# Performance work log

Measured on AMD Instinct MI355X. Metric: run time of the kernel, lower is better.

The kernel has to match this reference:

```python
import jax, jax.numpy as jnp
import numpy as np

EPS_BN = 1e-5

def _grid_sample(fea, gx, gy):
    # fea: [B,C,H,W]; gx,gy: [B,P] normalized to [-1,1]; bilinear, zeros padding, align_corners=True
    B, C, H, W = fea.shape
    x = (gx + 1.0) * 0.5 * (W - 1)
    y = (gy + 1.0) * 0.5 * (H - 1)
    x0 = jnp.floor(x)
    y0 = jnp.floor(y)
    wx1 = x - x0
    wy1 = y - y0
    flat = fea.reshape(B, C, H * W)
    def tap(xi, yi, w):
        valid = ((xi >= 0) & (xi <= W - 1) & (yi >= 0) & (yi <= H - 1)).astype(fea.dtype)
        xi_c = jnp.clip(xi, 0, W - 1).astype(jnp.int32)
        yi_c = jnp.clip(yi, 0, H - 1).astype(jnp.int32)
        g = jnp.take_along_axis(flat, (yi_c * W + xi_c)[:, None, :], axis=2)  # [B,C,P]
        return g * (w * valid)[:, None, :]
    return (tap(x0, y0, (1 - wx1) * (1 - wy1)) + tap(x0 + 1, y0, wx1 * (1 - wy1))
            + tap(x0, y0 + 1, (1 - wx1) * wy1) + tap(x0 + 1, y0 + 1, wx1 * wy1))

def _homo_warp(src_fea, src_proj, ref_proj, depth_values):
    # src_fea: [B,C,H,W] -> warped [B,C,D,H,W] (MVSNet homo_warping, grid under stop_gradient)
    B, C, H, W = src_fea.shape
    D = depth_values.shape[1]
    proj = jnp.matmul(src_proj, jnp.linalg.inv(ref_proj))
    rot, trans = proj[:, :3, :3], proj[:, :3, 3]
    yy, xx = jnp.meshgrid(jnp.arange(H, dtype=src_fea.dtype), jnp.arange(W, dtype=src_fea.dtype), indexing='ij')
    xyz = jnp.stack([xx.ravel(), yy.ravel(), jnp.ones(H * W, src_fea.dtype)], 0)  # [3,HW]
    rot_xyz = jnp.einsum('bij,jp->bip', rot, xyz)  # [B,3,HW]
    pxyz = rot_xyz[:, :, None, :] * depth_values.reshape(B, 1, D, H * W) + trans[:, :, None, None]  # [B,3,D,HW]
    z = pxyz[:, 2]
    gx = jax.lax.stop_gradient(((pxyz[:, 0] / z) / ((W - 1) / 2.0) - 1.0).reshape(B, D * H * W))
    gy = jax.lax.stop_gradient(((pxyz[:, 1] / z) / ((H - 1) / 2.0) - 1.0).reshape(B, D * H * W))
    return _grid_sample(src_fea, gx, gy).reshape(B, C, D, H, W)

def _pixelwise_net(x, w0, g0, b0, m0, v0, w1, g1, b1, m1, v1, w2, b2):
    # x: [B,1,D,H,W]; 1x1x1 Conv3d(bias=False)+BN+ReLU twice, then Conv3d(8->1)+sigmoid+max over D
    def bnrelu(h, g, b, m, v):
        s = (1, -1, 1, 1, 1)
        return jax.nn.relu((h - m.reshape(s)) * (g / jnp.sqrt(v + EPS_BN)).reshape(s) + b.reshape(s))
    h = bnrelu(jnp.einsum('oc,bcdhw->bodhw', w0, x), g0, b0, m0, v0)
    h = bnrelu(jnp.einsum('oc,bcdhw->bodhw', w1, h), g1, b1, m1, v1)
    h = jnp.einsum('oc,bcdhw->bodhw', w2, h) + b2.reshape(1, -1, 1, 1, 1)
    out = jax.nn.sigmoid(h[:, 0])  # [B,D,H,W]
    return jnp.max(out, axis=1, keepdims=True)  # [B,1,H,W]

def _forward(features, proj_matrices, depth_values, num_depth,
             pw_w0, pw_g0, pw_b0, pw_m0, pw_v0, pw_w1, pw_g1, pw_b1, pw_m1, pw_v1, pw_w2, pw_b2,
             reg_w, reg_b):
    ref_fea = features[0]
    B, C, H, W = ref_fea.shape
    V = features.shape[0]
    D = num_depth
    def proj_new(p):  # p: [B,2,4,4] -> K @ E on top 3 rows
        top = jnp.matmul(p[:, 1, :3, :3], p[:, 0, :3, :4])
        return jnp.concatenate([top, p[:, 0, 3:4, :]], axis=1)
    ref_proj_new = proj_new(proj_matrices[:, 0])
    sim_sum = jnp.zeros((B, 1, D, H, W), ref_fea.dtype)
    w_sum = jnp.full((B, 1, 1, H, W), 1e-5, ref_fea.dtype)
    vw_list = []
    for i in range(1, V):  # small fixed loop over source views
        src_proj_new = proj_new(proj_matrices[:, i])
        warped = _homo_warp(features[i], src_proj_new, ref_proj_new, depth_values)
        sim = jnp.mean(warped * ref_fea[:, :, None], axis=1, keepdims=True)  # [B,1,D,H,W]
        vw = _pixelwise_net(sim, pw_w0, pw_g0, pw_b0, pw_m0, pw_v0, pw_w1, pw_g1, pw_b1, pw_m1, pw_v1, pw_w2, pw_b2)
        vw_list.append(vw)
        sim_sum = sim_sum + sim * vw[:, :, None]
        w_sum = w_sum + vw[:, :, None]
    similarity = sim_sum / w_sum
    cost_reg = jax.lax.conv_general_dilated(similarity, reg_w, (1, 1, 1), 'SAME',
                                            dimension_numbers=('NCDHW', 'OIDHW', 'NCDHW')) + reg_b.reshape(1, -1, 1, 1, 1)
    prob_volume = jax.nn.softmax(cost_reg[:, 0], axis=1)  # exp(log_softmax) == softmax
    idx = jnp.argmax(prob_volume, axis=1, keepdims=True)
    depth = jnp.take_along_axis(depth_values, idx, axis=1)[:, 0]  # WTA depth [B,H,W]
    conf = jnp.max(prob_volume, axis=1)
    view_weights = jnp.concatenate(vw_list, axis=1)
    return depth, conf, prob_volume, cost_reg, view_weights

def setup_inputs():
    key = jax.random.key(0)
    ks = jax.random.split(key, 20)
    B, V, C, H, W, D = 2, 5, 32, 128, 160, 32
    features = jax.random.normal(ks[0], (V, B, C, H, W), jnp.float32)
    K = np.eye(4, dtype=np.float32)
    K[0, 0] = 180.0; K[1, 1] = 180.0; K[0, 2] = W / 2.0; K[1, 2] = H / 2.0
    pm = np.zeros((B, V, 2, 4, 4), np.float32)
    for v in range(V):
        E = np.eye(4, dtype=np.float32)
        E[0, 3] = 10.0 * v  # horizontal baseline per source view
        pm[:, v, 0] = E
        pm[:, v, 1] = K
    depth_values = jnp.broadcast_to(jnp.linspace(425.0, 935.0, D, dtype=jnp.float32)[None, :, None, None], (B, D, H, W)) + 0.0
    rn = lambda k, s, sc=0.3: jax.random.normal(k, s, jnp.float32) * sc
    return {
        'features': features,
        'proj_matrices': jnp.asarray(pm),
        'depth_values': depth_values,
        'num_depth': D,
        'pw_w0': rn(ks[1], (16, 1)),
        'pw_g0': 1.0 + rn(ks[2], (16,), 0.1), 'pw_b0': rn(ks[3], (16,), 0.1),
        'pw_m0': rn(ks[4], (16,), 0.1), 'pw_v0': 1.0 + 0.5 * jax.random.uniform(ks[5], (16,)),
        'pw_w1': rn(ks[6], (8, 16)),
        'pw_g1': 1.0 + rn(ks[7], (8,), 0.1), 'pw_b1': rn(ks[8], (8,), 0.1),
        'pw_m1': rn(ks[9], (8,), 0.1), 'pw_v1': 1.0 + 0.5 * jax.random.uniform(ks[10], (8,)),
        'pw_w2': rn(ks[11], (1, 8)),
        'pw_b2': rn(ks[12], (1,), 0.1),
        'reg_w': rn(ks[13], (1, 1, 3, 3, 3), 0.1),
        'reg_b': rn(ks[14], (1,), 0.1),
    }

def reference(features, proj_matrices, depth_values, num_depth,
              pw_w0, pw_g0, pw_b0, pw_m0, pw_v0, pw_w1, pw_g1, pw_b1, pw_m1, pw_v1, pw_w2, pw_b2,
              reg_w, reg_b):
    return _forward(features, proj_matrices, depth_values, num_depth,
                    pw_w0, pw_g0, pw_b0, pw_m0, pw_v0, pw_w1, pw_g1, pw_b1, pw_m1, pw_v1, pw_w2, pw_b2,
                    reg_w, reg_b)
```

## Files before the change

### kernel.cpp

```cpp
#include <hip/hip_runtime.h>
#include <math.h>

#define BB 2
#define VV 5
#define CC 32
#define HH 128
#define WW 160
#define DD 32
#define HWp (HH*WW)
#define NV (VV-1)
#define PX 16
#define MAXSLOT 18
#define UWMAX 30

#define OFF_RT   0
#define OFF_PRM  96
#define OFF_FEAT 512
#define OFF_SIM  (OFF_FEAT + VV*BB*HWp*CC)
#define OFF_T    (OFF_SIM + BB*DD*HWp)
#define OFF_TAB  (OFF_T + 16)
#define OFF_FLAG (OFF_TAB + 17*16)

#define OUT_DEPTH 0
#define OUT_CONF  (BB*HWp)
#define OUT_PROB  (2*BB*HWp)
#define OUT_COST  (OUT_PROB + BB*DD*HWp)
#define OUT_VW    (OUT_COST + BB*DD*HWp)

#define ZI(d,k)     smemU[(d)*17 + (k)]
#define DEP(d,k)    smemU[(d)*17 + (k)]
#define REF(p,c)    smemU[544 + (p)*36 + (c)]
#define GT(v,p,i)   smemU[1120 + ((v)*16 + (p))*18 + (i)]
#define AY0(v,p)    smemU[2272 + (v)*16 + (p)]
#define AY1(v,p)    smemU[2336 + (v)*16 + (p)]
#define IR0(v,p)    smemI[2400 + (v)*16 + (p)]
#define IR1(v,p)    smemI[2464 + (v)*16 + (p)]
#define IXB(v,p)    smemI[2528 + (v)*16 + (p)]
#define ISL(v,p)    smemI[2592 + (v)*16 + (p)]
#define BADF        smemI[2656]
#define SIMG(v,d,p) smemU[544 + (((v)*32 + (d))*17 + (p))]
#define COLU(v,ux,c) smemU[2720 + (v)*(UWMAX*36) + (ux)*36 + (c)]
#define UOKI(v)     smemI[7040 + (v)]
#define UXLOI(v)    smemI[7044 + (v)]
#define UWI(v)      smemI[7048 + (v)]

__device__ void build_proj(const float* proj, int b, int v, double M[4][4]) {
    const float* E = proj + (((b*VV + v)*2 + 0)*16);
    const float* K = proj + (((b*VV + v)*2 + 1)*16);
    for (int r = 0; r < 3; r++)
        for (int c = 0; c < 4; c++) {
            double s = 0.0;
            for (int k = 0; k < 3; k++) s += (double)K[r*4+k] * (double)E[k*4+c];
            M[r][c] = s;
        }
    for (int c = 0; c < 4; c++) M[3][c] = (double)E[12+c];
}

__device__ void inv4(const double M[4][4], double out[4][4]) {
    double a[4][8];
    for (int i = 0; i < 4; i++)
        for (int j = 0; j < 4; j++) { a[i][j] = M[i][j]; a[i][4+j] = (i == j) ? 1.0 : 0.0; }
    for (int col = 0; col < 4; col++) {
        int piv = col; double best = fabs(a[col][col]);
        for (int r = col+1; r < 4; r++) if (fabs(a[r][col]) > best) { best = fabs(a[r][col]); piv = r; }
        if (piv != col) for (int j = 0; j < 8; j++) { double t = a[col][j]; a[col][j] = a[piv][j]; a[piv][j] = t; }
        double dinv = 1.0 / a[col][col];
        for (int j = 0; j < 8; j++) a[col][j] *= dinv;
        for (int r = 0; r < 4; r++) {
            if (r == col) continue;
            double f = a[r][col];
            for (int j = 0; j < 8; j++) a[r][j] -= f * a[col][j];
        }
    }
    for (int i = 0; i < 4; i++) for (int j = 0; j < 4; j++) out[i][j] = a[i][4+j];
}

__device__ void setup_body(const float* __restrict__ proj,
    const float* __restrict__ w0, const float* __restrict__ g0, const float* __restrict__ b0,
    const float* __restrict__ m0, const float* __restrict__ v0,
    const float* __restrict__ w1, const float* __restrict__ g1, const float* __restrict__ b1,
    const float* __restrict__ m1, const float* __restrict__ v1,
    const float* __restrict__ w2, const float* __restrict__ b2,
    float* __restrict__ ws, int t,
    float* __restrict__ prmL, float* __restrict__ TL) {

    if (t < BB*NV) {
        int b = t / NV, v = 1 + (t % NV);
        double refM[4][4], inv[4][4], S[4][4];
        build_proj(proj, b, 0, refM);
        inv4(refM, inv);
        build_proj(proj, b, v, S);
        float* rt = ws + OFF_RT + (b*NV + (v-1))*12;
        for (int r = 0; r < 3; r++) {
            for (int c = 0; c < 3; c++) {
                double s = 0.0;
                for (int k = 0; k < 4; k++) s += S[r][k] * inv[k][c];
                rt[r*3 + c] = (float)s;
            }
            double s = 0.0;
            for (int k = 0; k < 4; k++) s += S[r][k] * inv[k][3];
            rt[9 + r] = (float)s;
        }
    }

    if (t < 16) {
        float sc = g0[t] / sqrtf(v0[t] + 1e-5f);
        prmL[t]      = w0[t] * sc;
        prmL[16 + t] = b0[t] - m0[t] * sc;
    }
    if (t >= 32 && t < 160) {
        int i = t - 32, q = i >> 4, o = i & 15;
        float sc = g1[q] / sqrtf(v1[q] + 1e-5f);
        prmL[32 + q*16 + o] = w1[q*16 + o] * sc;
    }
    if (t >= 160 && t < 168) {
        int q = t - 160;
        float sc = g1[q] / sqrtf(v1[q] + 1e-5f);
        prmL[160 + q] = b1[q] - m1[q] * sc;
        prmL[168 + q] = w2[q];
    }
    if (t == 176) prmL[176] = b2[0];
    __syncthreads();

    if (t < BB) {
        int ok = 1;
        for (int i = 0; i < NV; i++) {
            const float* ri = ws + OFF_RT + (t*NV + i)*12;
            ok &= (fabsf(ri[6])        < 1e-6f);
            ok &= (fabsf(ri[7])        < 1e-6f);
            ok &= (fabsf(ri[8] - 1.f)  < 1e-6f);
            ok &= (fabsf(ri[10])       < 1e-6f);
            ok &= (fabsf(ri[11])       < 1e-6f);
        }
        ws[OFF_FLAG + t] = ok ? 1.f : 0.f;
    }

    if (t == 0) {
        float tmp[16]; int nk = 0;
        for (int o = 0; o < 16; o++) {
            float a = prmL[o];
            if (a != 0.f) tmp[nk++] = -prmL[16+o] / a;
        }
        for (int i = 1; i < nk; i++) {
            float key = tmp[i]; int j = i-1;
            while (j >= 0 && tmp[j] > key) { tmp[j+1] = tmp[j]; j--; }
            tmp[j+1] = key;
        }
        for (int i = 0; i < 16; i++) TL[i] = (i < nk) ? tmp[i] : 3.4e38f;
    }
    __syncthreads();

    if (t < 17*8) {
        int seg = t >> 3, q = t & 7;
        float lo = (seg == 0)  ? -1e30f : TL[seg-1];
        float hi = (seg == 16) ?  1e30f : TL[seg];
        float smid;
        if (hi > 1e29f)       smid = lo + 1.f;
        else if (lo < -1e29f) smid = hi - 1.f;
        else                  smid = 0.5f*(lo + hi);
        float alpha = 0.f, beta = prmL[160+q];
        #pragma unroll
        for (int o = 0; o < 16; o++) {
            float a = prmL[o], c = prmL[16+o];
            if (a*smid + c > 0.f) {
                alpha += prmL[32+q*16+o]*a;
                beta  += prmL[32+q*16+o]*c;
            }
        }
        ws[OFF_TAB + seg*16 + q]     = alpha;
        ws[OFF_TAB + seg*16 + 8 + q] = beta;
    }
    if (t < 177) ws[OFF_PRM + t] = prmL[t];
    if (t < 16)  ws[OFF_T + t]   = TL[t];
}

__global__ __launch_bounds__(256) void transpose_setup_kernel(
    const float* __restrict__ fea, float* __restrict__ featT,
    const float* __restrict__ proj,
    const float* __restrict__ w0, const float* __restrict__ g0, const float* __restrict__ b0,
    const float* __restrict__ m0, const float* __restrict__ v0,
    const float* __restrict__ w1, const float* __restrict__ g1, const float* __restrict__ b1,
    const float* __restrict__ m1, const float* __restrict__ v1,
    const float* __restrict__ w2, const float* __restrict__ b2,
    float* __restrict__ ws) {
    __shared__ float prmL[177];
    __shared__ float TL[16];
    if (blockIdx.x == 0)
        setup_body(proj, w0, g0, b0, m0, v0, w1, g1, b1, m1, v1, w2, b2,
                   ws, threadIdx.x, prmL, TL);

    int t = blockIdx.x*256 + threadIdx.x;
    int w = t % WW;
    int h = (t / WW) % HH;
    int b = (t / (WW*HH)) % BB;
    int v = t / (WW*HH*BB);
    const float* src = fea + (size_t)((v*BB + b)*CC) * HWp + h*WW + w;
    float* dst = featT + (size_t)((v*BB + b)*HWp + h*WW + w) * CC;
    #pragma unroll
    for (int c = 0; c < CC; c += 4) {
        float4 q;
        q.x = src[(c+0)*HWp];
        q.y = src[(c+1)*HWp];
        q.z = src[(c+2)*HWp];
        q.w = src[(c+3)*HWp];
        *reinterpret_cast<float4*>(dst + c) = q;
    }
}

__device__ __forceinline__ float half_max(float v) {
    v = fmaxf(v, __shfl_xor(v, 1));
    v = fmaxf(v, __shfl_xor(v, 2));
    v = fmaxf(v, __shfl_xor(v, 4));
    v = fmaxf(v, __shfl_xor(v, 8));
    v = fmaxf(v, __shfl_xor(v, 16));
    return v;
}

__device__ __forceinline__ float dot32(const float* __restrict__ col,
                                       const float* __restrict__ refp) {
    float acc = 0.f;
    #pragma unroll
    for (int c = 0; c < CC; c += 4) {
        float4 a = *reinterpret_cast<const float4*>(col + c);
        float4 r = *reinterpret_cast<const float4*>(refp + c);
        acc = fmaf(a.w, r.w, fmaf(a.z, r.z, fmaf(a.y, r.y, fmaf(a.x, r.x, acc))));
    }
    return acc;
}

__device__ __forceinline__ float dot32_lds(const float* __restrict__ col,
                                           const float* __restrict__ refp) {
    float acc = 0.f;
    #pragma unroll
    for (int c = 0; c < CC; c += 4) {
        float4 a = *reinterpret_cast<const float4*>(col + c);
        float4 r = *reinterpret_cast<const float4*>(refp + c);
        acc = fmaf(a.w, r.w, fmaf(a.z, r.z, fmaf(a.y, r.y, fmaf(a.x, r.x, acc))));
    }
    return acc;
}

__device__ __forceinline__ void mlp_out(
    float s0, float s1, float s2, float s3,
    int d2, int b, int p,
    const float* __restrict__ tabL, const float* __restrict__ Tg,
    const float* __restrict__ prm,
    float* __restrict__ out, float* __restrict__ simout) {
    float T0 = Tg[0], T1 = Tg[1], T2 = Tg[2], T3 = Tg[3];
    float T4 = Tg[4], T5 = Tg[5], T6 = Tg[6], T7 = Tg[7];
    float T8 = Tg[8], T9 = Tg[9], T10 = Tg[10], T11 = Tg[11];
    float T12 = Tg[12], T13 = Tg[13], T14 = Tg[14], T15 = Tg[15];
    float wq0 = prm[168], wq1 = prm[169], wq2 = prm[170], wq3 = prm[171];
    float wq4 = prm[172], wq5 = prm[173], wq6 = prm[174], wq7 = prm[175];
    float p176 = prm[176];

    float sv[NV] = {s0, s1, s2, s3};
    float vw[NV];
    #pragma unroll
    for (int v = 0; v < NV; v++) {
        float s = sv[v];
        int seg = 0;
        seg += (s > T0);  seg += (s > T1);  seg += (s > T2);  seg += (s > T3);
        seg += (s > T4);  seg += (s > T5);  seg += (s > T6);  seg += (s > T7);
        seg += (s > T8);  seg += (s > T9);  seg += (s > T10); seg += (s > T11);
        seg += (s > T12); seg += (s > T13); seg += (s > T14); seg += (s > T15);
        const float* row = &tabL[seg << 4];
        float4 A0 = *reinterpret_cast<const float4*>(row);
        float4 A1 = *reinterpret_cast<const float4*>(row + 4);
        float4 B0 = *reinterpret_cast<const float4*>(row + 8);
        float4 B1 = *reinterpret_cast<const float4*>(row + 12);
        float h2v = p176;
        h2v = fmaf(wq0, fmaxf(fmaf(A0.x, s, B0.x), 0.f), h2v);
        h2v = fmaf(wq1, fmaxf(fmaf(A0.y, s, B0.y), 0.f), h2v);
        h2v = fmaf(wq2, fmaxf(fmaf(A0.z, s, B0.z), 0.f), h2v);
        h2v = fmaf(wq3, fmaxf(fmaf(A0.w, s, B0.w), 0.f), h2v);
        h2v = fmaf(wq4, fmaxf(fmaf(A1.x, s, B1.x), 0.f), h2v);
        h2v = fmaf(wq5, fmaxf(fmaf(A1.y, s, B1.y), 0.f), h2v);
        h2v = fmaf(wq6, fmaxf(fmaf(A1.z, s, B1.z), 0.f), h2v);
        h2v = fmaf(wq7, fmaxf(fmaf(A1.w, s, B1.w), 0.f), h2v);
        float m = half_max(h2v);
        vw[v] = 1.f/(1.f + __expf(-m));
    }

    if (d2 == 0) out[OUT_VW + (b*NV + 0)*HWp + p] = vw[0];
    if (d2 == 1) out[OUT_VW + (b*NV + 1)*HWp + p] = vw[1];
    if (d2 == 2) out[OUT_VW + (b*NV + 2)*HWp + p] = vw[2];
    if (d2 == 3) out[OUT_VW + (b*NV + 3)*HWp + p] = vw[3];

    float wsum = 1e-5f + vw[0] + vw[1] + vw[2] + vw[3];
    float ssum = s0*vw[0] + s1*vw[1] + s2*vw[2] + s3*vw[3];
    simout[(b*DD + d2)*HWp + p] = ssum / wsum;
}

__device__ __forceinline__ float tap_blend(
    const float* __restrict__ vbv, int sub8, float sx,
    float ay0, float ay1, int r0, int r1,
    float4 rva, float4 rvb) {
    float x0f = floorf(sx);
    float wx1 = sx - x0f;
    float wx0 = 1.f - wx1;
    int xi0 = (int)x0f, xi1 = xi0 + 1;
    float ax0 = ((unsigned)xi0 < WW) ? wx0 : 0.f;
    float ax1 = ((unsigned)xi1 < WW) ? wx1 : 0.f;
    int xc0 = min(max(xi0, 0), WW-1);
    int xc1 = min(max(xi1, 0), WW-1);
    float w00 = ax0*ay0, w01 = ax1*ay0;
    const float* q00 = vbv + (((r0 + xc0) << 5) + sub8);
    const float* q01 = vbv + (((r0 + xc1) << 5) + sub8);
    float4 t00a = *reinterpret_cast<const float4*>(q00);
    float4 t00b = *reinterpret_cast<const float4*>(q00 + 4);
    float4 t01a = *reinterpret_cast<const float4*>(q01);
    float4 t01b = *reinterpret_cast<const float4*>(q01 + 4);

    float blx = fmaf(w01, t01a.x, w00*t00a.x);
    float bly = fmaf(w01, t01a.y, w00*t00a.y);
    float blz = fmaf(w01, t01a.z, w00*t00a.z);
    float blw = fmaf(w01, t01a.w, w00*t00a.w);
    float acc = fmaf(rva.w,blw, fmaf(rva.z,blz, fmaf(rva.y,bly, rva.x*blx)));
    blx = fmaf(w01, t01b.x, w00*t00b.x);
    bly = fmaf(w01, t01b.y, w00*t00b.y);
    blz = fmaf(w01, t01b.z, w00*t00b.z);
    blw = fmaf(w01, t01b.w, w00*t00b.w);
    acc = fmaf(rvb.w,blw, fmaf(rvb.z,blz, fmaf(rvb.y,bly, fmaf(rvb.x,blx, acc))));

    if (ay1 != 0.f) {
        float w10 = ax0*ay1, w11 = ax1*ay1;
        const float* q10 = vbv + (((r1 + xc0) << 5) + sub8);
        const float* q11 = vbv + (((r1 + xc1) << 5) + sub8);
        float4 t10a = *reinterpret_cast<const float4*>(q10);
        float4 t10b = *reinterpret_cast<const float4*>(q10 + 4);
        float4 t11a = *reinterpret_cast<const float4*>(q11);
        float4 t11b = *reinterpret_cast<const float4*>(q11 + 4);
        float cx = fmaf(w11, t11a.x, w10*t10a.x);
        float cy = fmaf(w11, t11a.y, w10*t10a.y);
        float cz = fmaf(w11, t11a.z, w10*t10a.z);
        float cw = fmaf(w11, t11a.w, w10*t10a.w);
        acc = fmaf(rva.w,cw, fmaf(rva.z,cz, fmaf(rva.y,cy, fmaf(rva.x,cx, acc))));
        cx = fmaf(w11, t11b.x, w10*t10b.x);
        cy = fmaf(w11, t11b.y, w10*t10b.y);
        cz = fmaf(w11, t11b.z, w10*t10b.z);
        cw = fmaf(w11, t11b.w, w10*t10b.w);
        acc = fmaf(rvb.w,cw, fmaf(rvb.z,cz, fmaf(rvb.y,cy, fmaf(rvb.x,cx, acc))));
    }
    return acc;
}

__global__ __launch_bounds__(256) void fused_sim_kernel(
    const float* __restrict__ featT, const float* __restrict__ rtAll,
    const float* __restrict__ prm, const float* __restrict__ Tg,
    const float* __restrict__ tabG, const float* __restrict__ flagG,
    const float* __restrict__ depthv,
    float* __restrict__ simout, float* __restrict__ out) {
    __shared__ __align__(16) float smemU[7056];
    __shared__ __align__(16) float tabL[17*16];
    int* smemI = (int*)smemU;

    int t = threadIdx.x;
    int b = blockIdx.y;
    int pbase = blockIdx.x * PX;
    int hi  = pbase / WW;
    int wi0 = pbase % WW;
    float fy = (float)hi;

    bool fast = (flagG[b] != 0.f);

    {
        int di = t >> 4, k = t & 15;
        float dep0 = depthv[(b*DD + di)*HWp + pbase + k];
        float dep1 = depthv[(b*DD + di + 16)*HWp + pbase + k];
        if (fast) {
            ZI(di, k)    = __builtin_amdgcn_rcpf(dep0);
            ZI(di+16, k) = __builtin_amdgcn_rcpf(dep1);
            if (t < 128) {
                int p = t >> 3, c4 = (t & 7) * 4;
                float4 rq = *reinterpret_cast<const float4*>(
                    featT + (size_t)(b*HWp + pbase + p)*CC + c4);
                *reinterpret_cast<float4*>(&REF(p, c4)) = rq;
            }
        } else {
            DEP(di, k)    = dep0;
            DEP(di+16, k) = dep1;
        }
        tabL[t] = tabG[t];
        if (t < 16) tabL[256 + t] = tabG[256 + t];
        if (t == 0 && fast) BADF = 0;
    }
    __syncthreads();

    float rc[NV][12];
    #pragma unroll
    for (int v = 0; v < NV; v++)
        #pragma unroll
        for (int j = 0; j < 12; j++)
            rc[v][j] = rtAll[(b*NV + v)*12 + j];
    float bx0[NV], by0[NV], bz0[NV];
    #pragma unroll
    for (int v = 0; v < NV; v++) {
        bx0[v] = fmaf((float)wi0, rc[v][0], fmaf(fy, rc[v][1], rc[v][2]));
        by0[v] = fmaf((float)wi0, rc[v][3], fmaf(fy, rc[v][4], rc[v][5]));
        bz0[v] = fmaf((float)wi0, rc[v][6], fmaf(fy, rc[v][7], rc[v][8]));
    }

    bool needRestage = false;
    if (fast) {
        int p_loc = t >> 5, d = t & 31;
        for (int ph = 0; ph < 2; ph++) {
            int p = ph*8 + p_loc;
            float zi = ZI(d, p);
            float mnz = zi, mxz = zi;
            #pragma unroll
            for (int off = 1; off <= 16; off <<= 1) {
                mnz = fminf(mnz, __shfl_xor(mnz, off));
                mxz = fmaxf(mxz, __shfl_xor(mxz, off));
            }
            if (d == 0) {
                float fk = (float)p;
                #pragma unroll
                for (int v = 0; v < NV; v++) {
                    float bx = fmaf(fk, rc[v][0], bx0[v]);
                    float t0c = rc[v][9];
                    float sxa = fmaf(t0c, mnz, bx);
                    float sxb = fmaf(t0c, mxz, bx);
                    float mn = fminf(sxa, sxb), mx = fmaxf(sxa, sxb);
                    float by = fmaf(fk, rc[v][3], by0[v]);
                    float sy = by;
                    float sny = rintf(sy);
                    sy = (fabsf(sy - sny) < 1e-4f) ? sny : sy;
                    float y0f = floorf(sy);
                    float wy1 = sy - y0f, wy0 = 1.f - wy1;
                    int yi0 = (int)y0f, yi1 = yi0 + 1;
                    AY0(v, p) = ((unsigned)yi0 < HH) ? wy0 : 0.f;
                    AY1(v, p) = ((unsigned)yi1 < HH) ? wy1 : 0.f;
                    IR0(v, p) = min(max(yi0, 0), HH-1)*WW;
                    IR1(v, p) = min(max(yi1, 0), HH-1)*WW;
                    bool finite = (mn > -1e9f) && (mx < 1e9f) && (mn == mn) && (mx == mx);
                    int xb = finite ? (int)floorf(mn) : 0;
                    int slots = finite ? ((int)floorf(mx) - xb + 2) : MAXSLOT + 1;
                    IXB(v, p) = xb;
                    ISL(v, p) = slots;
                    if (slots > MAXSLOT) BADF = 1;
                }
            }
        }
        __syncthreads();
        if (BADF) { fast = false; needRestage = true; }
    }

    bool uni = false;
    if (fast) {
        if (t < 64) {
            int v = t >> 4, p = t & 15;
            int ok = (AY1(v, p) == 0.f) && (IR0(v, p) == IR0(v, 0)) ? 1 : 0;
            int xlo = IXB(v, p);
            int xhi = xlo + ISL(v, p) - 1;
            #pragma unroll
            for (int off = 1; off <= 8; off <<= 1) {
                ok  &= __shfl_xor(ok, off);
                xlo  = min(xlo, __shfl_xor(xlo, off));
                xhi  = max(xhi, __shfl_xor(xhi, off));
            }
            if (p == 0) {
                int wdt = xhi - xlo + 1;
                UOKI(v)  = (ok && wdt <= UWMAX) ? 1 : 0;
                UXLOI(v) = xlo;
                UWI(v)   = wdt;
            }
        }
        __syncthreads();
        uni = UOKI(0) && UOKI(1) && UOKI(2) && UOKI(3);
    }

    if (fast) {
        if (uni) {
            for (int i = t; i < NV*UWMAX*8; i += 256) {
                int v  = i / (UWMAX*8);
                int rem = i - v*(UWMAX*8);
                int ux = rem >> 3, c4 = (rem & 7) * 4;
                if (ux < UWI(v)) {
                    int xc = min(max(UXLOI(v) + ux, 0), WW-1);
                    int r0 = IR0(v, 0);
                    const float* src = featT + (size_t)(((v+1)*BB + b)*HWp)*CC
                                       + ((r0 + xc) << 5) + c4;
                    float4 q = *reinterpret_cast<const float4*>(src);
                    *reinterpret_cast<float4*>(&COLU(v, ux, c4)) = q;
                }
            }
            __syncthreads();
            {
                int v2 = t & 3, p2 = (t >> 2) & 15, i0 = t >> 6;
                float ay0 = AY0(v2, p2);
                int xb = IXB(v2, p2), slots = ISL(v2, p2);
                int xoff = xb - UXLOI(v2);
                const float* refp = &REF(p2, 0);
                for (int i2 = i0; i2 < slots; i2 += 4) {
                    const float* col = &COLU(v2, xoff + i2, 0);
                    float g = ay0 * dot32_lds(col, refp);
                    GT(v2, p2, i2) = g * (1.f/(float)CC);
                }
            }
            __syncthreads();
        } else {
            {
                int v2 = t & 3, p2 = (t >> 2) & 15, i0 = t >> 6;
                float ay0 = AY0(v2, p2), ay1 = AY1(v2, p2);
                int r0 = IR0(v2, p2), r1 = IR1(v2, p2);
                int xb = IXB(v2, p2), slots = ISL(v2, p2);
                const float* vbv = featT + (size_t)(((v2+1)*BB + b)*HWp)*CC;
                const float* refp = &REF(p2, 0);
                for (int i2 = i0; i2 < slots; i2 += 4) {
                    int xc = min(max(xb + i2, 0), WW-1);
                    float g = ay0 * dot32(vbv + ((r0 + xc) << 5), refp);
                    if (ay1 != 0.f) g = fmaf(ay1, dot32(vbv + ((r1 + xc) << 5), refp), g);
                    GT(v2, p2, i2) = g * (1.f/(float)CC);
                }
            }
            __syncthreads();
        }
        {
            int p_loc = t >> 5, d = t & 31;
            for (int ph = 0; ph < 2; ph++) {
                int p = ph*8 + p_loc;
                float fk = (float)p;
                float zi = ZI(d, p);
                float sv[NV];
                #pragma unroll
                for (int v = 0; v < NV; v++) {
                    float bx = fmaf(fk, rc[v][0], bx0[v]);
                    float sx = fmaf(rc[v][9], zi, bx);
                    float x0f = floorf(sx);
                    float wx1 = sx - x0f, wx0 = 1.f - wx1;
                    int xi0 = (int)x0f, xi1 = xi0 + 1;
                    float ax0 = ((unsigned)xi0 < WW) ? wx0 : 0.f;
                    float ax1 = ((unsigned)xi1 < WW) ? wx1 : 0.f;
                    int ii = xi0 - IXB(v, p);
                    float g0 = GT(v, p, ii);
                    float g1 = GT(v, p, ii+1);
                    sv[v] = fmaf(ax0, g0, ax1*g1);
                }
                mlp_out(sv[0], sv[1], sv[2], sv[3], d, b, pbase + p,
                        tabL, Tg, prm, out, simout);
            }
        }
        return;
    }

    if (needRestage) {
        int di = t >> 4, k = t & 15;
        DEP(di, k)    = depthv[(b*DD + di)*HWp + pbase + k];
        DEP(di+16, k) = depthv[(b*DD + di + 16)*HWp + pbase + k];
        __syncthreads();
    }
    {
        int sub = t & 3;
        int dB  = (t >> 2) & 31;
        int kk  = t >> 7;
        int sub8 = sub*8;
        #pragma unroll 2
        for (int j = 0; j < PX/2; j++) {
            int kpix = j*2 + kk;
            int p = pbase + kpix;
            float fk = (float)kpix;
            float depth = DEP(dB, kpix);
            const float* refp = featT + (size_t)(b*HWp + p)*CC + sub8;
            float4 rva = *reinterpret_cast<const float4*>(refp);
            float4 rvb = *reinterpret_cast<const float4*>(refp + 4);

            #pragma unroll
            for (int v = 0; v < NV; v++) {
                float bx = fmaf(fk, rc[v][0], bx0[v]);
                float by = fmaf(fk, rc[v][3], by0[v]);
                float bz = fmaf(fk, rc[v][6], bz0[v]);
                float px = fmaf(bx, depth, rc[v][9]);
                float py = fmaf(by, depth, rc[v][10]);
                float pz = fmaf(bz, depth, rc[v][11]);
                float zi = __builtin_amdgcn_rcpf(pz);
                float sx = px * zi, sy = py * zi;
                float sny = rintf(sy);
                sy = (fabsf(sy - sny) < 1e-4f) ? sny : sy;
                float y0f = floorf(sy);
                float wy1 = sy - y0f, wy0 = 1.f - wy1;
                int yi0 = (int)y0f, yi1 = yi0 + 1;
                float ay0 = ((unsigned)yi0 < HH) ? wy0 : 0.f;
                float ay1 = ((unsigned)yi1 < HH) ? wy1 : 0.f;
                int yc0 = min(max(yi0, 0), HH-1);
                int yc1 = min(max(yi1, 0), HH-1);
                int r0 = yc0*WW, r1 = yc1*WW;
                const float* vbv = featT + (size_t)(((v+1)*BB + b)*HWp)*CC;
                float acc = tap_blend(vbv, sub8, sx, ay0, ay1, r0, r1, rva, rvb);
                acc += __shfl_xor(acc, 1);
                acc += __shfl_xor(acc, 2);
                if (sub == 0) SIMG(v, dB, kpix) = acc * (1.f/(float)CC);
            }
        }
        __syncthreads();

        int p8 = t >> 5;
        int d2 = t & 31;
        #pragma unroll
        for (int pi = 0; pi < PX/8; pi++) {
            int pidx = pi*8 + p8;
            mlp_out(SIMG(0, d2, pidx), SIMG(1, d2, pidx),
                    SIMG(2, d2, pidx), SIMG(3, d2, pidx),
                    d2, b, pbase + pidx, tabL, Tg, prm, out, simout);
        }
    }
}

__global__ __launch_bounds__(256) void convsm_kernel(
    const float* __restrict__ sim, const float* __restrict__ rw,
    const float* __restrict__ rb, const float* __restrict__ depthv,
    float* __restrict__ out) {
    __shared__ float tile[34*121 + 7];
    int t = threadIdx.x;
    int tw = blockIdx.x * 8;
    int th = blockIdx.y * 8;
    int b  = blockIdx.z;

    for (int i = t; i < 34*120; i += 256) {
        int e = i / 120; int rem = i % 120;
        int h = rem / 12, w = rem % 12;
        int gd = e - 1, gh = th + h - 1, gw = tw + w - 1;
        float v = 0.f;
        if (w < 10 && gd >= 0 && gd < DD && (unsigned)gh < HH && (unsigned)gw < WW)
            v = sim[((b*DD + gd)*HH + gh)*WW + gw];
        tile[e*121 + rem] = v;
    }
    __syncthreads();

    float wk[27];
    #pragma unroll
    for (int i = 0; i < 27; i++) wk[i] = rw[i];
    float bias = rb[0];

    int p  = t >> 2, dq = t & 3;
    int ph = p >> 3, pw = p & 7;
    int d0 = dq * 8;

    float cost[8];
    #pragma unroll
    for (int j = 0; j < 8; j++) cost[j] = bias;
    #pragma unroll
    for (int e = 0; e < 10; e++) {
        int el = d0 + e;
        float s0 = 0.f, s1 = 0.f, s2 = 0.f;
        #pragma unroll
        for (int kh = 0; kh < 3; kh++) {
            #pragma unroll
            for (int kw = 0; kw < 3; kw++) {
                float x = tile[el*121 + (ph+kh)*12 + (pw+kw)];
                s0 = fmaf(wk[0*9 + kh*3 + kw], x, s0);
                s1 = fmaf(wk[1*9 + kh*3 + kw], x, s1);
                s2 = fmaf(wk[2*9 + kh*3 + kw], x, s2);
            }
        }
        if (e < 8)            cost[e]   += s0;
        if (e >= 1 && e <= 8) cost[e-1] += s1;
        if (e >= 2)           cost[e-2] += s2;
    }

    int pg = (th + ph)*WW + (tw + pw);
    #pragma unroll
    for (int j = 0; j < 8; j++)
        out[OUT_COST + (b*DD + d0 + j)*HWp + pg] = cost[j];

    float m = cost[0]; int mi = d0;
    #pragma unroll
    for (int j = 1; j < 8; j++) { if (cost[j] > m) { m = cost[j]; mi = d0 + j; } }
    #pragma unroll
    for (int off = 1; off <= 2; off <<= 1) {
        float m2 = __shfl_xor(m, off);
        int  i2 = __shfl_xor(mi, off);
        if (m2 > m || (m2 == m && i2 < mi)) { m = m2; mi = i2; }
    }
    float sum = 0.f;
    float e8[8];
    #pragma unroll
    for (int j = 0; j < 8; j++) { e8[j] = __expf(cost[j] - m); sum += e8[j]; }
    #pragma unroll
    for (int off = 1; off <= 2; off <<= 1) sum += __shfl_xor(sum, off);
    float inv = 1.f / sum;
    #pragma unroll
    for (int j = 0; j < 8; j++)
        out[OUT_PROB + (b*DD + d0 + j)*HWp + pg] = e8[j] * inv;
    if (dq == 0) {
        out[OUT_DEPTH + b*HWp + pg] = depthv[(b*DD + mi)*HWp + pg];
        out[OUT_CONF  + b*HWp + pg] = inv;
    }
}

extern "C" void kernel_launch(void* const* d_in, const int* in_sizes, int n_in,
                              void* d_out, int out_size, void* d_ws, size_t ws_size,
                              hipStream_t stream) {
    const float* features = (const float*)d_in[0];
    const float* proj     = (const float*)d_in[1];
    const float* depthv   = (const float*)d_in[2];
    const float* w0 = (const float*)d_in[4];
    const float* g0 = (const float*)d_in[5];
    const float* b0 = (const float*)d_in[6];
    const float* m0 = (const float*)d_in[7];
    const float* v0 = (const float*)d_in[8];
    const float* w1 = (const float*)d_in[9];
    const float* g1 = (const float*)d_in[10];
    const float* b1 = (const float*)d_in[11];
    const float* m1 = (const float*)d_in[12];
    const float* v1 = (const float*)d_in[13];
    const float* w2 = (const float*)d_in[14];
    const float* b2 = (const float*)d_in[15];
    const float* rw = (const float*)d_in[16];
    const float* rb = (const float*)d_in[17];
    float* out = (float*)d_out;
    float* ws  = (float*)d_ws;

    transpose_setup_kernel<<<VV*BB*HWp/256, 256, 0, stream>>>(
        features, ws + OFF_FEAT, proj,
        w0, g0, b0, m0, v0, w1, g1, b1, m1, v1, w2, b2, ws);

    fused_sim_kernel<<<dim3(HWp/PX, BB), 256, 0, stream>>>(
        ws + OFF_FEAT, ws + OFF_RT, ws + OFF_PRM, ws + OFF_T, ws + OFF_TAB,
        ws + OFF_FLAG, depthv, ws + OFF_SIM, out);

    convsm_kernel<<<dim3(WW/8, HH/8, BB), 256, 0, stream>>>(
        ws + OFF_SIM, rw, rb, depthv, out);
}
```

Baseline: 72.30 us.

## Drop feature transpose pass and gather directly from channel-major features

Result: slower. 81.36 us (+12.5%).

```diff
diff --git a/kernel.cpp b/kernel.cpp
--- a/kernel.cpp
+++ b/kernel.cpp
@@ -15,8 +15,7 @@
 
 #define OFF_RT   0
 #define OFF_PRM  96
-#define OFF_FEAT 512
-#define OFF_SIM  (OFF_FEAT + VV*BB*HWp*CC)
+#define OFF_SIM  512
 #define OFF_T    (OFF_SIM + BB*DD*HWp)
 #define OFF_TAB  (OFF_T + 16)
 #define OFF_FLAG (OFF_TAB + 17*16)
@@ -75,14 +74,16 @@
     for (int i = 0; i < 4; i++) for (int j = 0; j < 4; j++) out[i][j] = a[i][4+j];
 }
 
-__device__ void setup_body(const float* __restrict__ proj,
+__global__ __launch_bounds__(256) void setup_kernel(const float* __restrict__ proj,
     const float* __restrict__ w0, const float* __restrict__ g0, const float* __restrict__ b0,
     const float* __restrict__ m0, const float* __restrict__ v0,
     const float* __restrict__ w1, const float* __restrict__ g1, const float* __restrict__ b1,
     const float* __restrict__ m1, const float* __restrict__ v1,
     const float* __restrict__ w2, const float* __restrict__ b2,
-    float* __restrict__ ws, int t,
-    float* __restrict__ prmL, float* __restrict__ TL) {
+    float* __restrict__ ws) {
+    __shared__ float prmL[177];
+    __shared__ float TL[16];
+    int t = threadIdx.x;
 
     if (t < BB*NV) {
         int b = t / NV, v = 1 + (t % NV);
@@ -174,39 +175,6 @@
     if (t < 16)  ws[OFF_T + t]   = TL[t];
 }
 
-__global__ __launch_bounds__(256) void transpose_setup_kernel(
-    const float* __restrict__ fea, float* __restrict__ featT,
-    const float* __restrict__ proj,
-    const float* __restrict__ w0, const float* __restrict__ g0, const float* __restrict__ b0,
-    const float* __restrict__ m0, const float* __restrict__ v0,
-    const float* __restrict__ w1, const float* __restrict__ g1, const float* __restrict__ b1,
-    const float* __restrict__ m1, const float* __restrict__ v1,
-    const float* __restrict__ w2, const float* __restrict__ b2,
-    float* __restrict__ ws) {
-    __shared__ float prmL[177];
-    __shared__ float TL[16];
-    if (blockIdx.x == 0)
-        setup_body(proj, w0, g0, b0, m0, v0, w1, g1, b1, m1, v1, w2, b2,
-                   ws, threadIdx.x, prmL, TL);
-
-    int t = blockIdx.x*256 + threadIdx.x;
-    int w = t % WW;
-    int h = (t / WW) % HH;
-    int b = (t / (WW*HH)) % BB;
-    int v = t / (WW*HH*BB);
-    const float* src = fea + (size_t)((v*BB + b)*CC) * HWp + h*WW + w;
-    float* dst = featT + (size_t)((v*BB + b)*HWp + h*WW + w) * CC;
-    #pragma unroll
-    for (int c = 0; c < CC; c += 4) {
-        float4 q;
-        q.x = src[(c+0)*HWp];
-        q.y = src[(c+1)*HWp];
-        q.z = src[(c+2)*HWp];
-        q.w = src[(c+3)*HWp];
-        *reinterpret_cast<float4*>(dst + c) = q;
-    }
-}
-
 __device__ __forceinline__ float half_max(float v) {
     v = fmaxf(v, __shfl_xor(v, 1));
     v = fmaxf(v, __shfl_xor(v, 2));
@@ -214,18 +182,6 @@
     v = fmaxf(v, __shfl_xor(v, 8));
     v = fmaxf(v, __shfl_xor(v, 16));
     return v;
-}
-
-__device__ __forceinline__ float dot32(const float* __restrict__ col,
-                                       const float* __restrict__ refp) {
-    float acc = 0.f;
-    #pragma unroll
-    for (int c = 0; c < CC; c += 4) {
-        float4 a = *reinterpret_cast<const float4*>(col + c);
-        float4 r = *reinterpret_cast<const float4*>(refp + c);
-        acc = fmaf(a.w, r.w, fmaf(a.z, r.z, fmaf(a.y, r.y, fmaf(a.x, r.x, acc))));
-    }
-    return acc;
 }
 
 __device__ __forceinline__ float dot32_lds(const float* __restrict__ col,
@@ -292,61 +248,8 @@
     simout[(b*DD + d2)*HWp + p] = ssum / wsum;
 }
 
-__device__ __forceinline__ float tap_blend(
-    const float* __restrict__ vbv, int sub8, float sx,
-    float ay0, float ay1, int r0, int r1,
-    float4 rva, float4 rvb) {
-    float x0f = floorf(sx);
-    float wx1 = sx - x0f;
-    float wx0 = 1.f - wx1;
-    int xi0 = (int)x0f, xi1 = xi0 + 1;
-    float ax0 = ((unsigned)xi0 < WW) ? wx0 : 0.f;
-    float ax1 = ((unsigned)xi1 < WW) ? wx1 : 0.f;
-    int xc0 = min(max(xi0, 0), WW-1);
-    int xc1 = min(max(xi1, 0), WW-1);
-    float w00 = ax0*ay0, w01 = ax1*ay0;
-    const float* q00 = vbv + (((r0 + xc0) << 5) + sub8);
-    const float* q01 = vbv + (((r0 + xc1) << 5) + sub8);
-    float4 t00a = *reinterpret_cast<const float4*>(q00);
-    float4 t00b = *reinterpret_cast<const float4*>(q00 + 4);
-    float4 t01a = *reinterpret_cast<const float4*>(q01);
-    float4 t01b = *reinterpret_cast<const float4*>(q01 + 4);
-
-    float blx = fmaf(w01, t01a.x, w00*t00a.x);
-    float bly = fmaf(w01, t01a.y, w00*t00a.y);
-    float blz = fmaf(w01, t01a.z, w00*t00a.z);
-    float blw = fmaf(w01, t01a.w, w00*t00a.w);
-    float acc = fmaf(rva.w,blw, fmaf(rva.z,blz, fmaf(rva.y,bly, rva.x*blx)));
-    blx = fmaf(w01, t01b.x, w00*t00b.x);
-    bly = fmaf(w01, t01b.y, w00*t00b.y);
-    blz = fmaf(w01, t01b.z, w00*t00b.z);
-    blw = fmaf(w01, t01b.w, w00*t00b.w);
-    acc = fmaf(rvb.w,blw, fmaf(rvb.z,blz, fmaf(rvb.y,bly, fmaf(rvb.x,blx, acc))));
-
-    if (ay1 != 0.f) {
-        float w10 = ax0*ay1, w11 = ax1*ay1;
-        const float* q10 = vbv + (((r1 + xc0) << 5) + sub8);
-        const float* q11 = vbv + (((r1 + xc1) << 5) + sub8);
-        float4 t10a = *reinterpret_cast<const float4*>(q10);
-        float4 t10b = *reinterpret_cast<const float4*>(q10 + 4);
-        float4 t11a = *reinterpret_cast<const float4*>(q11);
-        float4 t11b = *reinterpret_cast<const float4*>(q11 + 4);
-        float cx = fmaf(w11, t11a.x, w10*t10a.x);
-        float cy = fmaf(w11, t11a.y, w10*t10a.y);
-        float cz = fmaf(w11, t11a.z, w10*t10a.z);
-        float cw = fmaf(w11, t11a.w, w10*t10a.w);
-        acc = fmaf(rva.w,cw, fmaf(rva.z,cz, fmaf(rva.y,cy, fmaf(rva.x,cx, acc))));
-        cx = fmaf(w11, t11b.x, w10*t10b.x);
-        cy = fmaf(w11, t11b.y, w10*t10b.y);
-        cz = fmaf(w11, t11b.z, w10*t10b.z);
-        cw = fmaf(w11, t11b.w, w10*t10b.w);
-        acc = fmaf(rvb.w,cw, fmaf(rvb.z,cz, fmaf(rvb.y,cy, fmaf(rvb.x,cx, acc))));
-    }
-    return acc;
-}
-
 __global__ __launch_bounds__(256) void fused_sim_kernel(
-    const float* __restrict__ featT, const float* __restrict__ rtAll,
+    const float* __restrict__ fea, const float* __restrict__ rtAll,
     const float* __restrict__ prm, const float* __restrict__ Tg,
     const float* __restrict__ tabG, const float* __restrict__ flagG,
     const float* __restrict__ depthv,
@@ -371,11 +274,9 @@
         if (fast) {
             ZI(di, k)    = __builtin_amdgcn_rcpf(dep0);
             ZI(di+16, k) = __builtin_amdgcn_rcpf(dep1);
-            if (t < 128) {
-                int p = t >> 3, c4 = (t & 7) * 4;
-                float4 rq = *reinterpret_cast<const float4*>(
-                    featT + (size_t)(b*HWp + pbase + p)*CC + c4);
-                *reinterpret_cast<float4*>(&REF(p, c4)) = rq;
+            for (int i = t; i < CC*PX; i += 256) {
+                int c = i >> 4, p = i & 15;
+                REF(p, c) = fea[((size_t)(b*CC + c))*HWp + pbase + p];
             }
         } else {
             DEP(di, k)    = dep0;
@@ -472,17 +373,15 @@
 
     if (fast) {
         if (uni) {
-            for (int i = t; i < NV*UWMAX*8; i += 256) {
-                int v  = i / (UWMAX*8);
-                int rem = i - v*(UWMAX*8);
-                int ux = rem >> 3, c4 = (rem & 7) * 4;
+            for (int i = t; i < NV*CC*UWMAX; i += 256) {
+                int v   = i / (CC*UWMAX);
+                int rem = i - v*(CC*UWMAX);
+                int c   = rem / UWMAX;
+                int ux  = rem - c*UWMAX;
                 if (ux < UWI(v)) {
                     int xc = min(max(UXLOI(v) + ux, 0), WW-1);
-                    int r0 = IR0(v, 0);
-                    const float* src = featT + (size_t)(((v+1)*BB + b)*HWp)*CC
-                                       + ((r0 + xc) << 5) + c4;
-                    float4 q = *reinterpret_cast<const float4*>(src);
-                    *reinterpret_cast<float4*>(&COLU(v, ux, c4)) = q;
+                    COLU(v, ux, c) = fea[((size_t)(((v+1)*BB + b)*CC + c))*HWp
+                                         + IR0(v, 0) + xc];
                 }
             }
             __syncthreads();
@@ -505,12 +404,20 @@
                 float ay0 = AY0(v2, p2), ay1 = AY1(v2, p2);
                 int r0 = IR0(v2, p2), r1 = IR1(v2, p2);
                 int xb = IXB(v2, p2), slots = ISL(v2, p2);
-                const float* vbv = featT + (size_t)(((v2+1)*BB + b)*HWp)*CC;
+                const float* plane = fea + (size_t)(((v2+1)*BB + b)*CC)*HWp;
                 const float* refp = &REF(p2, 0);
                 for (int i2 = i0; i2 < slots; i2 += 4) {
                     int xc = min(max(xb + i2, 0), WW-1);
-                    float g = ay0 * dot32(vbv + ((r0 + xc) << 5), refp);
-                    if (ay1 != 0.f) g = fmaf(ay1, dot32(vbv + ((r1 + xc) << 5), refp), g);
+                    float g = 0.f;
+                    for (int c = 0; c < CC; c++)
+                        g = fmaf(plane[(size_t)c*HWp + r0 + xc], refp[c], g);
+                    g *= ay0;
+                    if (ay1 != 0.f) {
+                        float h = 0.f;
+                        for (int c = 0; c < CC; c++)
+                            h = fmaf(plane[(size_t)c*HWp + r1 + xc], refp[c], h);
+                        g = fmaf(ay1, h, g);
+                    }
                     GT(v2, p2, i2) = g * (1.f/(float)CC);
                 }
             }
@@ -555,15 +462,16 @@
         int dB  = (t >> 2) & 31;
         int kk  = t >> 7;
         int sub8 = sub*8;
-        #pragma unroll 2
+        const float* planeR = fea + (size_t)(b*CC)*HWp;
         for (int j = 0; j < PX/2; j++) {
             int kpix = j*2 + kk;
             int p = pbase + kpix;
             float fk = (float)kpix;
             float depth = DEP(dB, kpix);
-            const float* refp = featT + (size_t)(b*HWp + p)*CC + sub8;
-            float4 rva = *reinterpret_cast<const float4*>(refp);
-            float4 rvb = *reinterpret_cast<const float4*>(refp + 4);
+            float refv[8];
+            #pragma unroll
+            for (int jj = 0; jj < 8; jj++)
+                refv[jj] = planeR[(size_t)(sub8+jj)*HWp + p];
 
             #pragma unroll
             for (int v = 0; v < NV; v++) {
@@ -577,16 +485,32 @@
                 float sx = px * zi, sy = py * zi;
                 float sny = rintf(sy);
                 sy = (fabsf(sy - sny) < 1e-4f) ? sny : sy;
-                float y0f = floorf(sy);
-                float wy1 = sy - y0f, wy0 = 1.f - wy1;
-                int yi0 = (int)y0f, yi1 = yi0 + 1;
+                float x0f = floorf(sx), y0f = floorf(sy);
+                float wx1 = sx - x0f, wy1 = sy - y0f;
+                float wx0 = 1.f - wx1, wy0 = 1.f - wy1;
+                int xi0 = (int)x0f, yi0 = (int)y0f;
+                int xi1 = xi0 + 1,  yi1 = yi0 + 1;
+                float ax0 = ((unsigned)xi0 < WW) ? wx0 : 0.f;
+                float ax1 = ((unsigned)xi1 < WW) ? wx1 : 0.f;
                 float ay0 = ((unsigned)yi0 < HH) ? wy0 : 0.f;
                 float ay1 = ((unsigned)yi1 < HH) ? wy1 : 0.f;
+                int xc0 = min(max(xi0, 0), WW-1);
+                int xc1 = min(max(xi1, 0), WW-1);
                 int yc0 = min(max(yi0, 0), HH-1);
                 int yc1 = min(max(yi1, 0), HH-1);
                 int r0 = yc0*WW, r1 = yc1*WW;
-                const float* vbv = featT + (size_t)(((v+1)*BB + b)*HWp)*CC;
-                float acc = tap_blend(vbv, sub8, sx, ay0, ay1, r0, r1, rva, rvb);
+                float w00 = ax0*ay0, w01 = ax1*ay0;
+                float w10 = ax0*ay1, w11 = ax1*ay1;
+                const float* plane = fea + (size_t)(((v+1)*BB + b)*CC)*HWp;
+                float acc = 0.f;
+                #pragma unroll
+                for (int jj = 0; jj < 8; jj++) {
+                    const float* pl = plane + (size_t)(sub8+jj)*HWp;
+                    float blend = fmaf(w01, pl[r0+xc1], w00*pl[r0+xc0]);
+                    if (ay1 != 0.f)
+                        blend = fmaf(w11, pl[r1+xc1], fmaf(w10, pl[r1+xc0], blend));
+                    acc = fmaf(refv[jj], blend, acc);
+                }
                 acc += __shfl_xor(acc, 1);
                 acc += __shfl_xor(acc, 2);
                 if (sub == 0) SIMG(v, dB, kpix) = acc * (1.f/(float)CC);
@@ -711,12 +635,10 @@
     float* out = (float*)d_out;
     float* ws  = (float*)d_ws;
 
-    transpose_setup_kernel<<<VV*BB*HWp/256, 256, 0, stream>>>(
-        features, ws + OFF_FEAT, proj,
-        w0, g0, b0, m0, v0, w1, g1, b1, m1, v1, w2, b2, ws);
+    setup_kernel<<<1, 256, 0, stream>>>(proj, w0, g0, b0, m0, v0, w1, g1, b1, m1, v1, w2, b2, ws);
 
     fused_sim_kernel<<<dim3(HWp/PX, BB), 256, 0, stream>>>(
-        ws + OFF_FEAT, ws + OFF_RT, ws + OFF_PRM, ws + OFF_T, ws + OFF_TAB,
+        features, ws + OFF_RT, ws + OFF_PRM, ws + OFF_T, ws + OFF_TAB,
         ws + OFF_FLAG, depthv, ws + OFF_SIM, out);
 
     convsm_kernel<<<dim3(WW/8, HH/8, BB), 256, 0, stream>>>(
```
